# Performance work log

Measured on AMD Instinct MI355X. Metric: run time of the kernel, lower is better.

Reference implementation:

```python
import jax, jax.numpy as jnp
import numpy as np

Q_DIM, KV_DIM, H = 64, 64, 4


def setup_inputs() -> dict:
    key = jax.random.key(0)
    ks = jax.random.split(key, 8)
    b, t = 8, 128
    q_x = jax.random.normal(ks[0], (b, t, Q_DIM), dtype=jnp.float32)
    kv_x = jax.random.normal(ks[1], (b, t, t - 1, KV_DIM), dtype=jnp.float32)
    # nn.Linear weights: (out_features, in_features), applied as x @ W.T
    Wk = jax.random.normal(ks[2], (KV_DIM * H, KV_DIM), dtype=jnp.float32) * 0.05
    Wq = jax.random.normal(ks[3], (KV_DIM * H, Q_DIM), dtype=jnp.float32) * 0.05
    Wv = jax.random.normal(ks[4], (KV_DIM * H, KV_DIM), dtype=jnp.float32) * 0.05
    bias = jax.random.uniform(ks[5], (KV_DIM,), minval=-0.1, maxval=0.1, dtype=jnp.float32)
    Ws = jax.random.normal(ks[6], (1, KV_DIM), dtype=jnp.float32) * 0.05
    bs = jax.random.normal(ks[7], (1,), dtype=jnp.float32) * 0.05
    return {"q_x": q_x, "kv_x": kv_x, "Wk": Wk, "Wq": Wq, "Wv": Wv,
            "bias": bias, "Ws": Ws, "bs": bs}


def reference(q_x, kv_x, Wk, Wq, Wv, bias, Ws, bs):
    b, t, tm1, k = kv_x.shape  # tm1 == t-1
    h = H
    # keys: (b, t, t-1, h, k)
    keys = (kv_x @ Wk.T).reshape(b, t, tm1, h, k)
    # queries: (b, t, 1, h, k)
    queries = (q_x @ Wq.T).reshape(b, t, 1, h, k)
    # additive tanh score projected to scalar per (b,t,n,h)
    act = jnp.tanh(keys + queries + bias)
    score = jnp.einsum('btnhk,k->btnh', act, Ws[0]) + bs[0]
    # softmax over the t-1 key axis (dim=2)
    w = jax.nn.softmax(score, axis=2)  # (b, t, t-1, h)
    values = (kv_x @ Wv.T).reshape(b, t, tm1, h, k)
    # weighted sum over t-1
    x = jnp.einsum('btnh,btnhk->bthk', w, values)
    return x.reshape(b, t, h * k)
```

## Files before the change

kernel.cpp:

```cpp
#include <hip/hip_runtime.h>
#include <math.h>

#define B 8
#define T 128
#define NKEY 127
#define KDIM 64
#define NH 4
#define CH 256

typedef _Float16 half8 __attribute__((ext_vector_type(8)));
typedef float floatx4 __attribute__((ext_vector_type(4)));

__device__ __forceinline__ float fast_tanh(float x) {
    float e = __expf(2.f * x);
    float r = __builtin_amdgcn_rcpf(e + 1.f);
    return fmaf(-2.f, r, 1.f);
}

__device__ __forceinline__ half8 cvt8(const float4& a, const float4& b) {
    half8 h;
    h[0] = (_Float16)a.x; h[1] = (_Float16)a.y;
    h[2] = (_Float16)a.z; h[3] = (_Float16)a.w;
    h[4] = (_Float16)b.x; h[5] = (_Float16)b.y;
    h[6] = (_Float16)b.z; h[7] = (_Float16)b.w;
    return h;
}

__global__ __launch_bounds__(512, 8)
void attn_kernel(const float* __restrict__ q_x,
                 const float* __restrict__ kv_x,
                 const float* __restrict__ Wk,
                 const float* __restrict__ Wq,
                 const float* __restrict__ Wv,
                 const float* __restrict__ bias,
                 const float* __restrict__ Ws,
                 const float* __restrict__ bs,
                 float* __restrict__ out)
{
    __shared__ __align__(16) _Float16 bh_lds[16][64][8];
    __shared__ __align__(16) float qb_lds[CH];
    __shared__ __align__(16) float pp_lds[8][128];

    float* const probs = (float*)bh_lds;
    float* const wkv2  = (float*)bh_lds + 512;

    const int bt   = blockIdx.x;
    const int tid  = threadIdx.x;
    const int wid  = tid >> 6;
    const int lane = tid & 63;
    const int col  = lane & 15;
    const int quad = lane >> 4;
    const int h    = wid & 3;
    const int role = wid >> 2;

    const float* __restrict__ kvg = kv_x + (size_t)bt * NKEY * KDIM;

    #pragma unroll
    for (int w = 0; w < 2; ++w) {
        const int chunk = w * 8 + wid;
        const int nt = chunk >> 1, ks = chunk & 1;
        const int n  = nt * 16 + col;
        const int k0 = ks * 32 + quad * 8;
        float4 a = make_float4(0.f, 0.f, 0.f, 0.f);
        float4 b = make_float4(0.f, 0.f, 0.f, 0.f);
        if (n < NKEY) {
            const float* p = kvg + (size_t)n * KDIM + k0;
            a = *(const float4*)p;
            b = *(const float4*)(p + 4);
        }
        *(half8*)&bh_lds[chunk][lane][0] = cvt8(a, b);
    }

    half8 ah[2][2];
    #pragma unroll
    for (int jtl = 0; jtl < 2; ++jtl)
        #pragma unroll
        for (int ks = 0; ks < 2; ++ks) {
            const float* wrow = Wk + (size_t)(h * 64 + role * 32 + jtl * 16 + col) * KDIM
                                   + ks * 32 + quad * 8;
            float4 a = *(const float4*)wrow;
            float4 b = *(const float4*)(wrow + 4);
            ah[jtl][ks] = cvt8(a, b);
        }

    {
        const int c = tid >> 1, kh = tid & 1;
        const float4* Wq4 = (const float4*)(Wq + (size_t)c * KDIM + kh * 32);
        const float4* q4g = (const float4*)(q_x + (size_t)bt * KDIM + kh * 32);
        float4 qa = make_float4(0.f, 0.f, 0.f, 0.f);
        #pragma unroll
        for (int i = 0; i < 8; ++i) {
            float4 w = Wq4[i];
            float4 q4 = q4g[i];
            qa.x = fmaf(q4.x, w.x, qa.x);
            qa.y = fmaf(q4.y, w.y, qa.y);
            qa.z = fmaf(q4.z, w.z, qa.z);
            qa.w = fmaf(q4.w, w.w, qa.w);
        }
        float r = (qa.x + qa.y) + (qa.z + qa.w);
        r += __shfl_xor(r, 1, 64);
        if (kh == 0) qb_lds[c] = r + bias[c & 63];
    }

    __syncthreads();

    floatx4 qb4[2];
    float4  wsv[2];
    #pragma unroll
    for (int jtl = 0; jtl < 2; ++jtl) {
        qb4[jtl] = *(const floatx4*)&qb_lds[h * 64 + role * 32 + jtl * 16 + quad * 4];
        wsv[jtl] = *(const float4*)&Ws[role * 32 + jtl * 16 + quad * 4];
    }

    #pragma unroll
    for (int nt = 0; nt < 8; ++nt) {
        half8 b0 = *(const half8*)&bh_lds[nt * 2 + 0][lane][0];
        half8 b1 = *(const half8*)&bh_lds[nt * 2 + 1][lane][0];
        float partial = 0.f;
        #pragma unroll
        for (int jtl = 0; jtl < 2; ++jtl) {
            floatx4 c = qb4[jtl];
            c = __builtin_amdgcn_mfma_f32_16x16x32_f16(ah[jtl][0], b0, c, 0, 0, 0);
            c = __builtin_amdgcn_mfma_f32_16x16x32_f16(ah[jtl][1], b1, c, 0, 0, 0);
            #pragma unroll
            for (int r = 0; r < 4; ++r)
                partial = fmaf(fast_tanh(c[r]), wsv[jtl][r], partial);
        }
        partial += __shfl_xor(partial, 16, 64);
        partial += __shfl_xor(partial, 32, 64);
        if (lane < 16) pp_lds[wid][nt * 16 + lane] = partial;
    }

    __syncthreads();

    float invl;
    {
        float s_a = pp_lds[h][lane]      + pp_lds[4 + h][lane];
        float s_b = pp_lds[h][64 + lane] + pp_lds[4 + h][64 + lane];
        if (lane == 63) s_b = -1e30f;
        float mx = fmaxf(s_a, s_b);
        #pragma unroll
        for (int off = 32; off > 0; off >>= 1)
            mx = fmaxf(mx, __shfl_xor(mx, off, 64));
        float pa = __expf(s_a - mx);
        float pb = __expf(s_b - mx);
        float ls = pa + pb;
        #pragma unroll
        for (int off = 32; off > 0; off >>= 1)
            ls += __shfl_xor(ls, off, 64);
        invl = 1.f / ls;
        if (role == 0) {
            probs[h * 128 + lane]      = pa;
            probs[h * 128 + 64 + lane] = pb;
        }
    }

    __syncthreads();

    {
        const float* kvl = kvg + lane;
        const float* pr  = probs + h * 128;
        const int n0 = role * 64;
        float w0 = 0.f, w1 = 0.f, w2 = 0.f, w3 = 0.f;
        #pragma unroll 4
        for (int n4 = n0; n4 < n0 + 64; n4 += 4) {
            float4 p4 = *(const float4*)&pr[n4];
            const int n3 = (n4 + 3 < NKEY) ? (n4 + 3) : 0;
            w0 = fmaf(p4.x, kvl[(size_t)(n4 + 0) * KDIM], w0);
            w1 = fmaf(p4.y, kvl[(size_t)(n4 + 1) * KDIM], w1);
            w2 = fmaf(p4.z, kvl[(size_t)(n4 + 2) * KDIM], w2);
            w3 = fmaf(p4.w, kvl[(size_t)n3 * KDIM], w3);
        }
        wkv2[wid * 64 + lane] = ((w0 + w1) + (w2 + w3)) * invl;
    }

    __syncthreads();

    {
        const int c = tid >> 1, kh = tid & 1;
        const int hc = c >> 6;
        const float4* wa  = (const float4*)&wkv2[hc * 64 + kh * 32];
        const float4* wb  = (const float4*)&wkv2[(4 + hc) * 64 + kh * 32];
        const float4* Wv4 = (const float4*)(Wv + (size_t)c * KDIM + kh * 32);
        float4 oa = make_float4(0.f, 0.f, 0.f, 0.f);
        #pragma unroll
        for (int i = 0; i < 8; ++i) {
            float4 w = Wv4[i];
            float4 v = wa[i];
            float4 u = wb[i];
            oa.x = fmaf(v.x + u.x, w.x, oa.x);
            oa.y = fmaf(v.y + u.y, w.y, oa.y);
            oa.z = fmaf(v.z + u.z, w.z, oa.z);
            oa.w = fmaf(v.w + u.w, w.w, oa.w);
        }
        float r = (oa.x + oa.y) + (oa.z + oa.w);
        r += __shfl_xor(r, 1, 64);
        if (kh == 0) out[(size_t)bt * CH + c] = r;
    }
}

extern "C" void kernel_launch(void* const* d_in, const int* in_sizes, int n_in,
                              void* d_out, int out_size, void* d_ws, size_t ws_size,
                              hipStream_t stream) {
    const float* q_x  = (const float*)d_in[0];
    const float* kv_x = (const float*)d_in[1];
    const float* Wk   = (const float*)d_in[2];
    const float* Wq   = (const float*)d_in[3];
    const float* Wv   = (const float*)d_in[4];
    const float* bias = (const float*)d_in[5];
    const float* Ws   = (const float*)d_in[6];
    const float* bs   = (const float*)d_in[7];
    float* out = (float*)d_out;

    attn_kernel<<<dim3(B * T), dim3(512), 0, stream>>>(
        q_x, kv_x, Wk, Wq, Wv, bias, Ws, bs, out);
}
```

Before: 123.1 us.

## Stage kv tile in LDS via direct global-to-LDS loads and reuse it

Loads the fp32 kv tile straight into shared memory with global_load_lds, converting to fp16 only when building the MFMA operands. The same LDS tile then feeds the probability-weighted sum, which replaces the second global read of kv_x, the probs LDS buffer and one barrier with shuffle broadcasts. The tanh-score accumulation is also rewritten algebraically as sum(Ws) plus -2·Ws·rcp(e+1), dropping one FMA per element. The trade-off is roughly doubled LDS per block, which may lower occupancy, plus round-toward-zero fp16 conversion of kv.

```diff
diff --git a/kernel.cpp b/kernel.cpp
--- a/kernel.cpp
+++ b/kernel.cpp
@@ -9,15 +9,29 @@
 #define CH 256
 
 typedef _Float16 half8 __attribute__((ext_vector_type(8)));
+typedef __fp16 fp16x2 __attribute__((ext_vector_type(2)));
 typedef float floatx4 __attribute__((ext_vector_type(4)));
 
-__device__ __forceinline__ float fast_tanh(float x) {
-    float e = __expf(2.f * x);
-    float r = __builtin_amdgcn_rcpf(e + 1.f);
-    return fmaf(-2.f, r, 1.f);
-}
-
-__device__ __forceinline__ half8 cvt8(const float4& a, const float4& b) {
+typedef __attribute__((address_space(1))) const unsigned GBuf;
+typedef __attribute__((address_space(3))) unsigned LBuf;
+__device__ __forceinline__ void gload_lds16(const void* g, void* lds) {
+    __builtin_amdgcn_global_load_lds((GBuf*)g, (LBuf*)lds, 16, 0, 0);
+}
+
+__device__ __forceinline__ half8 cvt8_rtz(const float4& a, const float4& b) {
+    fp16x2 p0 = __builtin_amdgcn_cvt_pkrtz(a.x, a.y);
+    fp16x2 p1 = __builtin_amdgcn_cvt_pkrtz(a.z, a.w);
+    fp16x2 p2 = __builtin_amdgcn_cvt_pkrtz(b.x, b.y);
+    fp16x2 p3 = __builtin_amdgcn_cvt_pkrtz(b.z, b.w);
+    half8 h;
+    h[0] = (_Float16)p0[0]; h[1] = (_Float16)p0[1];
+    h[2] = (_Float16)p1[0]; h[3] = (_Float16)p1[1];
+    h[4] = (_Float16)p2[0]; h[5] = (_Float16)p2[1];
+    h[6] = (_Float16)p3[0]; h[7] = (_Float16)p3[1];
+    return h;
+}
+
+__device__ __forceinline__ half8 cvt8_rne(const float4& a, const float4& b) {
     half8 h;
     h[0] = (_Float16)a.x; h[1] = (_Float16)a.y;
     h[2] = (_Float16)a.z; h[3] = (_Float16)a.w;
@@ -37,12 +51,10 @@
                  const float* __restrict__ bs,
                  float* __restrict__ out)
 {
-    __shared__ __align__(16) _Float16 bh_lds[16][64][8];
+    __shared__ __align__(16) float kv_lds[128][64];
     __shared__ __align__(16) float qb_lds[CH];
     __shared__ __align__(16) float pp_lds[8][128];
-
-    float* const probs = (float*)bh_lds;
-    float* const wkv2  = (float*)bh_lds + 512;
+    __shared__ __align__(16) float wkv2[8][64];
 
     const int bt   = blockIdx.x;
     const int tid  = threadIdx.x;
@@ -55,20 +67,15 @@
 
     const float* __restrict__ kvg = kv_x + (size_t)bt * NKEY * KDIM;
 
-    #pragma unroll
-    for (int w = 0; w < 2; ++w) {
-        const int chunk = w * 8 + wid;
-        const int nt = chunk >> 1, ks = chunk & 1;
-        const int n  = nt * 16 + col;
-        const int k0 = ks * 32 + quad * 8;
-        float4 a = make_float4(0.f, 0.f, 0.f, 0.f);
-        float4 b = make_float4(0.f, 0.f, 0.f, 0.f);
-        if (n < NKEY) {
-            const float* p = kvg + (size_t)n * KDIM + k0;
-            a = *(const float4*)p;
-            b = *(const float4*)(p + 4);
-        }
-        *(half8*)&bh_lds[chunk][lane][0] = cvt8(a, b);
+    {
+        const char* gb = (const char*)kvg;
+        #pragma unroll
+        for (int w = 0; w < 4; ++w) {
+            const int idx = wid * 4 + w;
+            int off = idx * 1024 + lane * 16;
+            off = (off >= NKEY * 256) ? off - 256 : off;
+            gload_lds16(gb + off, &kv_lds[idx * 4][0]);
+        }
     }
 
     half8 ah[2][2];
@@ -80,7 +87,7 @@
                                    + ks * 32 + quad * 8;
             float4 a = *(const float4*)wrow;
             float4 b = *(const float4*)(wrow + 4);
-            ah[jtl][ks] = cvt8(a, b);
+            ah[jtl][ks] = cvt8_rne(a, b);
         }
 
     {
@@ -105,26 +112,38 @@
     __syncthreads();
 
     floatx4 qb4[2];
-    float4  wsv[2];
+    float4  ws2[2];
+    float   wssum = 0.f;
     #pragma unroll
     for (int jtl = 0; jtl < 2; ++jtl) {
         qb4[jtl] = *(const floatx4*)&qb_lds[h * 64 + role * 32 + jtl * 16 + quad * 4];
-        wsv[jtl] = *(const float4*)&Ws[role * 32 + jtl * 16 + quad * 4];
+        float4 w = *(const float4*)&Ws[role * 32 + jtl * 16 + quad * 4];
+        wssum += (w.x + w.y) + (w.z + w.w);
+        ws2[jtl] = make_float4(-2.f * w.x, -2.f * w.y, -2.f * w.z, -2.f * w.w);
     }
 
     #pragma unroll
     for (int nt = 0; nt < 8; ++nt) {
-        half8 b0 = *(const half8*)&bh_lds[nt * 2 + 0][lane][0];
-        half8 b1 = *(const half8*)&bh_lds[nt * 2 + 1][lane][0];
-        float partial = 0.f;
+        const float* krow = &kv_lds[nt * 16 + col][quad * 8];
+        float4 f0 = *(const float4*)(krow);
+        float4 f1 = *(const float4*)(krow + 4);
+        float4 f2 = *(const float4*)(krow + 32);
+        float4 f3 = *(const float4*)(krow + 36);
+        half8 b0 = cvt8_rtz(f0, f1);
+        half8 b1 = cvt8_rtz(f2, f3);
+
+        float partial = wssum;
         #pragma unroll
         for (int jtl = 0; jtl < 2; ++jtl) {
             floatx4 c = qb4[jtl];
             c = __builtin_amdgcn_mfma_f32_16x16x32_f16(ah[jtl][0], b0, c, 0, 0, 0);
             c = __builtin_amdgcn_mfma_f32_16x16x32_f16(ah[jtl][1], b1, c, 0, 0, 0);
             #pragma unroll
-            for (int r = 0; r < 4; ++r)
-                partial = fmaf(fast_tanh(c[r]), wsv[jtl][r], partial);
+            for (int r = 0; r < 4; ++r) {
+                float e  = __expf(2.f * c[r]);
+                float rc = __builtin_amdgcn_rcpf(e + 1.f);
+                partial  = fmaf((&ws2[jtl].x)[r], rc, partial);
+            }
         }
         partial += __shfl_xor(partial, 16, 64);
         partial += __shfl_xor(partial, 32, 64);
@@ -133,7 +152,7 @@
 
     __syncthreads();
 
-    float invl;
+    float pa, pb, invl;
     {
         float s_a = pp_lds[h][lane]      + pp_lds[4 + h][lane];
         float s_b = pp_lds[h][64 + lane] + pp_lds[4 + h][64 + lane];
@@ -142,36 +161,38 @@
         #pragma unroll
         for (int off = 32; off > 0; off >>= 1)
             mx = fmaxf(mx, __shfl_xor(mx, off, 64));
-        float pa = __expf(s_a - mx);
-        float pb = __expf(s_b - mx);
+        pa = __expf(s_a - mx);
+        pb = __expf(s_b - mx);
         float ls = pa + pb;
         #pragma unroll
         for (int off = 32; off > 0; off >>= 1)
             ls += __shfl_xor(ls, off, 64);
         invl = 1.f / ls;
-        if (role == 0) {
-            probs[h * 128 + lane]      = pa;
-            probs[h * 128 + 64 + lane] = pb;
-        }
-    }
-
-    __syncthreads();
-
-    {
-        const float* kvl = kvg + lane;
-        const float* pr  = probs + h * 128;
-        const int n0 = role * 64;
-        float w0 = 0.f, w1 = 0.f, w2 = 0.f, w3 = 0.f;
-        #pragma unroll 4
-        for (int n4 = n0; n4 < n0 + 64; n4 += 4) {
-            float4 p4 = *(const float4*)&pr[n4];
-            const int n3 = (n4 + 3 < NKEY) ? (n4 + 3) : 0;
-            w0 = fmaf(p4.x, kvl[(size_t)(n4 + 0) * KDIM], w0);
-            w1 = fmaf(p4.y, kvl[(size_t)(n4 + 1) * KDIM], w1);
-            w2 = fmaf(p4.z, kvl[(size_t)(n4 + 2) * KDIM], w2);
-            w3 = fmaf(p4.w, kvl[(size_t)n3 * KDIM], w3);
-        }
-        wkv2[wid * 64 + lane] = ((w0 + w1) + (w2 + w3)) * invl;
+    }
+
+    {
+        const float ps = role ? pb : pa;
+        const int   c4 = (lane & 15) * 4;
+        floatx4 acc = {0.f, 0.f, 0.f, 0.f};
+        #pragma unroll
+        for (int i = 0; i < 16; ++i) {
+            float p  = __shfl(ps, i * 4 + quad, 64);
+            float4 v = *(const float4*)&kv_lds[role * 64 + i * 4 + quad][c4];
+            acc[0] = fmaf(p, v.x, acc[0]);
+            acc[1] = fmaf(p, v.y, acc[1]);
+            acc[2] = fmaf(p, v.z, acc[2]);
+            acc[3] = fmaf(p, v.w, acc[3]);
+        }
+        #pragma unroll
+        for (int k = 0; k < 4; ++k) {
+            acc[k] += __shfl_xor(acc[k], 16, 64);
+            acc[k] += __shfl_xor(acc[k], 32, 64);
+        }
+        if (lane < 16) {
+            float4 o = make_float4(acc[0] * invl, acc[1] * invl,
+                                   acc[2] * invl, acc[3] * invl);
+            *(float4*)&wkv2[wid][c4] = o;
+        }
     }
 
     __syncthreads();
@@ -179,8 +200,8 @@
     {
         const int c = tid >> 1, kh = tid & 1;
         const int hc = c >> 6;
-        const float4* wa  = (const float4*)&wkv2[hc * 64 + kh * 32];
-        const float4* wb  = (const float4*)&wkv2[(4 + hc) * 64 + kh * 32];
+        const float4* wa  = (const float4*)&wkv2[hc][kh * 32];
+        const float4* wb  = (const float4*)&wkv2[4 + hc][kh * 32];
         const float4* Wv4 = (const float4*)(Wv + (size_t)c * KDIM + kh * 32);
         float4 oa = make_float4(0.f, 0.f, 0.f, 0.f);
         #pragma unroll
```

Result: slower. 126.4 us (+2.6%).
